# Kernel tuning notes

Measured on AMD Instinct MI355X. Metric: run time of the kernel, lower is better.

## Reference

```python
import jax, jax.numpy as jnp
import numpy as np
from jax import lax

SCALE = 2
KSIZE = 5
RGB_RANGE = 255.0
RGB_MEAN = (0.4488, 0.4371, 0.404)


def setup_inputs() -> dict:
    key = jax.random.key(0)
    ks = jax.random.split(key, 8)
    N, C, H, W = 4, 3, 128, 128
    G0 = 64
    s = SCALE
    x = jax.random.normal(ks[0], (N, C, H, W), dtype=jnp.float32)
    # relative position matrix: (1, (H*s)*(W*s), 3), values in [0,1)
    pos_mat = jax.random.uniform(ks[1], (1, H * s * W * s, 3), dtype=jnp.float32)
    conv_w = jax.random.normal(ks[2], (G0, C, KSIZE, KSIZE), dtype=jnp.float32) * 0.05
    conv_b = jax.random.normal(ks[3], (G0,), dtype=jnp.float32) * 0.05
    w1 = jax.random.normal(ks[4], (3, 256), dtype=jnp.float32) * 0.05
    b1 = jax.random.normal(ks[5], (256,), dtype=jnp.float32) * 0.05
    w2 = jax.random.normal(ks[6], (256, 9 * G0 * 3), dtype=jnp.float32) * 0.05
    b2 = jax.random.normal(ks[7], (9 * G0 * 3,), dtype=jnp.float32) * 0.05
    return {"x": x, "pos_mat": pos_mat, "conv_w": conv_w, "conv_b": conv_b,
            "w1": w1, "b1": b1, "w2": w2, "b2": b2}


def _unfold3(feat):
    # torch F.unfold(feat, 3, padding=1) ordering: channel-major then (ki, kj)
    N, C, H, W = feat.shape
    p = jnp.pad(feat, ((0, 0), (0, 0), (1, 1), (1, 1)))
    patches = jnp.stack([p[:, :, i:i + H, j:j + W]
                         for i in range(3) for j in range(3)], axis=2)  # [N,C,9,H,W]
    return patches.reshape(N, C * 9, H * W)  # [N, C*9, L]


def reference(x, pos_mat, conv_w, conv_b, w1, b1, w2, b2):
    s = SCALE
    N, _, H, W = x.shape
    # Feature extraction: conv5x5 (SAME) + ReLU
    feat = lax.conv_general_dilated(x, conv_w, (1, 1), 'SAME',
                                    dimension_numbers=('NCHW', 'OIHW', 'NCHW'))
    feat = jax.nn.relu(feat + conv_b[None, :, None, None])  # [N, G0, H, W]
    G0 = feat.shape[1]
    K = G0 * 9
    # Pos2Weight MLP: per output-pixel dynamic conv weights
    p = pos_mat.reshape(-1, 3)  # [(H*s)*(W*s), 3]
    lw = jax.nn.relu(p @ w1 + b1) @ w2 + b2  # [(H*s)*(W*s), K*3]
    # reshape to [s^2, H*W, K, 3] matching torch permute pipeline
    lw = lw.reshape(H, s, W, s, K, 3).transpose(1, 3, 0, 2, 4, 5).reshape(s * s, H * W, K, 3)
    # unfold 3x3 patches (repeat_x just tiles identical copies; compute once)
    cols = _unfold3(feat).transpose(0, 2, 1)  # [N, L, K], L = H*W
    # per-pixel matmul: out[n,p,l,c] = sum_k cols[n,l,k] * lw[p,l,k,c]
    out = jnp.einsum('nlk,plkc->nplc', cols, lw)  # [N, s^2, L, 3]
    # pixel-shuffle style rearrangement to [N, 3, H*s, W*s]
    out = out.reshape(N, s, s, H, W, 3).transpose(0, 5, 3, 1, 4, 2)
    out = out.reshape(N, 3, H * s, W * s)
    # add_mean (MeanShift sign=+1, std=1)
    mean = jnp.asarray(RGB_MEAN, dtype=out.dtype) * RGB_RANGE
    return out + mean[None, :, None, None]
```

## Files before the change

kernel.cpp:

```cpp
#include <hip/hip_runtime.h>

#define HW   128
#define OHW  256
#define G0n  64
#define HID  256
#define NOUT 1728
#define NB   4

typedef __attribute__((ext_vector_type(8))) short bf16x8;
typedef __attribute__((ext_vector_type(4))) float f32x4;
typedef __attribute__((ext_vector_type(4))) unsigned int u32x4;
typedef __attribute__((ext_vector_type(2))) unsigned int u32x2;

__device__ __forceinline__ unsigned short f2bf(float f) {
    unsigned int u = __builtin_bit_cast(unsigned int, f);
    u += 0x7fffu + ((u >> 16) & 1u);
    return (unsigned short)(u >> 16);
}
__device__ __forceinline__ float bflo(unsigned int d) {
    return __builtin_bit_cast(float, d << 16);
}
__device__ __forceinline__ float bfhi(unsigned int d) {
    return __builtin_bit_cast(float, d & 0xffff0000u);
}

__global__ __launch_bounds__(256) void prep_w2t(const float* __restrict__ w2,
                                                unsigned short* __restrict__ w2t) {
    __shared__ float t[64][65];
    int kb = blockIdx.x & 3, cb = blockIdx.x >> 2;
    int lc = threadIdx.x & 63, lr = threadIdx.x >> 6;
    #pragma unroll
    for (int i = 0; i < 16; ++i) {
        int kk = lr + i * 4;
        t[kk][lc] = w2[(kb * 64 + kk) * NOUT + cb * 64 + lc];
    }
    __syncthreads();
    #pragma unroll
    for (int i = 0; i < 16; ++i) {
        int cc = lr + i * 4;
        w2t[(cb * 64 + cc) * 256 + kb * 64 + lc] = f2bf(t[lc][cc]);
    }
}

__global__ __launch_bounds__(256) void conv5_relu_kernel(
    const float* __restrict__ x, const float* __restrict__ cw,
    const float* __restrict__ cb, float* __restrict__ feat)
{
    int idx = blockIdx.x * 256 + threadIdx.x;
    int w4 = (idx & 31) * 4;
    int h  = (idx >> 5) & 127;
    int g  = (idx >> 12) & 63;
    int n  = idx >> 18;
    float bv = cb[g];
    float a[4] = {bv, bv, bv, bv};
    const float* wp = cw + g * 75;
    #pragma unroll
    for (int ci = 0; ci < 3; ++ci) {
        const float* xr = x + (n * 3 + ci) * (HW * HW);
        #pragma unroll
        for (int ki = 0; ki < 5; ++ki) {
            int hh = h + ki - 2;
            if (hh < 0 || hh >= HW) continue;
            const float* row = xr + hh * HW;
            float f[8];
            if (w4 != 0 && w4 != 124) {
                float2 u0 = *(const float2*)(row + w4 - 2);
                float2 u1 = *(const float2*)(row + w4);
                float2 u2 = *(const float2*)(row + w4 + 2);
                float2 u3 = *(const float2*)(row + w4 + 4);
                f[0] = u0.x; f[1] = u0.y; f[2] = u1.x; f[3] = u1.y;
                f[4] = u2.x; f[5] = u2.y; f[6] = u3.x; f[7] = u3.y;
            } else {
                #pragma unroll
                for (int j = 0; j < 8; ++j) {
                    int ww = w4 - 2 + j;
                    f[j] = (ww >= 0 && ww < HW) ? row[ww] : 0.0f;
                }
            }
            float wt[5];
            #pragma unroll
            for (int kj = 0; kj < 5; ++kj) wt[kj] = wp[ci * 25 + ki * 5 + kj];
            #pragma unroll
            for (int j = 0; j < 4; ++j)
                #pragma unroll
                for (int kj = 0; kj < 5; ++kj)
                    a[j] = fmaf(f[j + kj], wt[kj], a[j]);
        }
    }
    float4 o;
    o.x = fmaxf(a[0], 0.f); o.y = fmaxf(a[1], 0.f);
    o.z = fmaxf(a[2], 0.f); o.w = fmaxf(a[3], 0.f);
    *(float4*)&feat[((n * G0n + g) * HW + h) * HW + w4] = o;
}

__global__ __launch_bounds__(256, 2) void fused_metasr_mfma(
    const float* __restrict__ feat, const unsigned short* __restrict__ w2t,
    const float* __restrict__ pos,  const float* __restrict__ w1,
    const float* __restrict__ b1,   const float* __restrict__ b2,
    float* __restrict__ out)
{
    __shared__ __align__(16) unsigned short AL[64 * 260];
    __shared__ __align__(16) unsigned short FT[64 * 6 * 4 * 8];

    const int tid = threadIdx.x;
    const int bx = blockIdx.x & 31, by = blockIdx.x >> 5;
    const int oy0 = by * 8, ox0 = bx * 8;
    const int h0 = by * 4,  w0 = bx * 4;

    for (int i = tid; i < 64 * 6 * 4 * 8; i += 256) {
        int c  = i & 7;
        int n  = (i >> 3) & 3;
        int r  = (i >> 5) % 6;
        int ci = (i >> 5) / 6;
        int gh = h0 - 1 + r, gw = w0 - 1 + c;
        float v = 0.0f;
        if (c < 6 && gh >= 0 && gh < HW && gw >= 0 && gw < HW)
            v = feat[((n * G0n + ci) * HW + gh) * HW + gw];
        FT[i] = f2bf(v);
    }

    {
        int px = tid >> 2, q = tid & 3;
        int rr = (oy0 + (px >> 3)) * OHW + (ox0 + (px & 7));
        float p0 = pos[rr * 3 + 0], p1 = pos[rr * 3 + 1], p2 = pos[rr * 3 + 2];
        #pragma unroll
        for (int j = 0; j < 16; ++j) {
            int k0 = q * 4 + j * 16;
            float4 wa = *(const float4*)&w1[k0];
            float4 wb = *(const float4*)&w1[HID + k0];
            float4 wc = *(const float4*)&w1[2 * HID + k0];
            float4 bb = *(const float4*)&b1[k0];
            unsigned short h0s = f2bf(fmaxf(fmaf(p0, wa.x, fmaf(p1, wb.x, fmaf(p2, wc.x, bb.x))), 0.f));
            unsigned short h1s = f2bf(fmaxf(fmaf(p0, wa.y, fmaf(p1, wb.y, fmaf(p2, wc.y, bb.y))), 0.f));
            unsigned short h2s = f2bf(fmaxf(fmaf(p0, wa.z, fmaf(p1, wb.z, fmaf(p2, wc.z, bb.z))), 0.f));
            unsigned short h3s = f2bf(fmaxf(fmaf(p0, wa.w, fmaf(p1, wb.w, fmaf(p2, wc.w, bb.w))), 0.f));
            u32x2 pk;
            pk.x = (unsigned)h0s | ((unsigned)h1s << 16);
            pk.y = (unsigned)h2s | ((unsigned)h3s << 16);
            *(u32x2*)&AL[px * 260 + k0] = pk;
        }
    }
    __syncthreads();

    const int lane = tid & 63, nq = tid >> 6;
    const int cl = lane & 15, hi = lane >> 4;
    bf16x8 afrag[4][8];
    #pragma unroll
    for (int m = 0; m < 4; ++m)
        #pragma unroll
        for (int k8 = 0; k8 < 8; ++k8)
            afrag[m][k8] = *(const bf16x8*)&AL[(m * 16 + cl) * 260 + k8 * 32 + hi * 8];

    const int epx = tid >> 2, en = tid & 3;
    const int iy = (epx >> 3) >> 1;
    const int ix = (epx & 7) >> 1;
    const bool selhi = (ix >= 2);
    const bool podd  = (ix & 1) != 0;
    const unsigned lwbase = (unsigned)(epx * 520);
    float oacc0 = 0.f, oacc1 = 0.f, oacc2 = 0.f;

    for (int ch = 0; ch < 9; ++ch) {
        f32x4 acc[4][3];
        #pragma unroll
        for (int m = 0; m < 4; ++m)
            #pragma unroll
            for (int j = 0; j < 3; ++j)
                acc[m][j] = (f32x4){0.f, 0.f, 0.f, 0.f};

        #pragma unroll
        for (int kh = 0; kh < 2; ++kh) {
            #pragma unroll
            for (int kk = 0; kk < 4; ++kk) {
                bf16x8 bfrag[3];
                #pragma unroll
                for (int j = 0; j < 3; ++j) {
                    int col = nq * 48 + j * 16 + cl;
                    bfrag[j] = *(const bf16x8*)&w2t[(ch * 192 + col) * 256 + kh * 128 + kk * 32 + hi * 8];
                }
                #pragma unroll
                for (int m = 0; m < 4; ++m)
                    #pragma unroll
                    for (int j = 0; j < 3; ++j)
                        acc[m][j] = __builtin_amdgcn_mfma_f32_16x16x32_bf16(
                            afrag[m][kh * 4 + kk], bfrag[j], acc[m][j], 0, 0, 0);
            }
        }

        __syncthreads();
        #pragma unroll
        for (int j = 0; j < 3; ++j) {
            int col = nq * 48 + j * 16 + cl;
            float bv = b2[ch * 192 + col];
            int kt = col / 3;
            int c  = col - kt * 3;
            #pragma unroll
            for (int m = 0; m < 4; ++m)
                #pragma unroll
                for (int r = 0; r < 4; ++r) {
                    int row = m * 16 + hi * 4 + r;
                    AL[row * 260 + kt * 4 + c] = f2bf(acc[m][j][r] + bv);
                }
        }
        __syncthreads();

        int k0 = ch * 64;
        int t3a = k0 / 3;
        int t3b = (k0 + 63) / 3;
        auto do_t3 = [&](int t3, bool guard) {
            int ci = t3 / 3;
            int di = t3 - ci * 3;
            const char* fp = (const char*)FT + ci * 384 + (iy + di) * 64 + en * 16;
            u32x4 w = *(const u32x4*)fp;
            unsigned a0 = selhi ? w.y : w.x;
            unsigned b0 = selhi ? w.z : w.y;
            float loa = bflo(a0), hia = bfhi(a0);
            float lob = bflo(b0), hib = bfhi(b0);
            float f0 = podd ? hia : loa;
            float f1 = podd ? lob : hia;
            float f2 = podd ? hib : lob;
            int ktb = 3 * t3 - k0;
            #pragma unroll
            for (int dj = 0; dj < 3; ++dj) {
                int kt = ktb + dj;
                float fv = dj == 0 ? f0 : (dj == 1 ? f1 : f2);
                if (guard) {
                    fv = ((unsigned)kt < 64u) ? fv : 0.0f;
                    kt = kt < 0 ? 0 : (kt > 63 ? 63 : kt);
                }
                u32x2 d = *(const u32x2*)((const char*)AL + lwbase + (unsigned)(kt * 8));
                oacc0 = fmaf(fv, bflo(d.x), oacc0);
                oacc1 = fmaf(fv, bfhi(d.x), oacc1);
                oacc2 = fmaf(fv, bflo(d.y), oacc2);
            }
        };
        do_t3(t3a, true);
        for (int t3 = t3a + 1; t3 < t3b; ++t3) do_t3(t3, false);
        do_t3(t3b, true);
    }

    int oy = oy0 + (epx >> 3), ox = ox0 + (epx & 7);
    out[((en * 3 + 0) * OHW + oy) * OHW + ox] = oacc0 + 0.4488f * 255.0f;
    out[((en * 3 + 1) * OHW + oy) * OHW + ox] = oacc1 + 0.4371f * 255.0f;
    out[((en * 3 + 2) * OHW + oy) * OHW + ox] = oacc2 + 0.4040f * 255.0f;
}

extern "C" void kernel_launch(void* const* d_in, const int* in_sizes, int n_in,
                              void* d_out, int out_size, void* d_ws, size_t ws_size,
                              hipStream_t stream) {
    (void)in_sizes; (void)n_in; (void)out_size; (void)ws_size;
    const float* x      = (const float*)d_in[0];
    const float* posm   = (const float*)d_in[1];
    const float* conv_w = (const float*)d_in[2];
    const float* conv_b = (const float*)d_in[3];
    const float* w1     = (const float*)d_in[4];
    const float* b1     = (const float*)d_in[5];
    const float* w2     = (const float*)d_in[6];
    const float* b2     = (const float*)d_in[7];
    float* out = (float*)d_out;

    unsigned short* w2t = (unsigned short*)d_ws;
    float* feat = (float*)((char*)d_ws + 884736);

    prep_w2t<<<108, 256, 0, stream>>>(w2, w2t);
    conv5_relu_kernel<<<(NB * G0n * HW * 32) / 256, 256, 0, stream>>>(x, conv_w, conv_b, feat);
    fused_metasr_mfma<<<1024, 256, 0, stream>>>(feat, w2t, posm, w1, b1, b2, out);
}
```

Measured before the change: 235.1 us.

## Warp-specialize fused MetaSR kernel into MFMA producer and consumer waves

Doubles the block to 512 threads. Four waves run the MFMA weight-generation GEMM and four consumer waves apply the per-pixel dynamic weights, using double-buffered LDS (AL0/AL1) so chunk ch+1's GEMM overlaps chunk ch's consumption. The feature tile is now loaded per chunk into a double-buffered slice instead of all at once, and B-fragment global loads are software-prefetched with raised wave priority around the MFMAs. This aims to hide the serialized GEMM/epilogue phases, at the cost of more LDS per block (possibly lower occupancy) and a barrier every chunk.

New measurement: 273.4 us. 1.16x slower.

```diff
diff --git a/kernel.cpp b/kernel.cpp
--- a/kernel.cpp
+++ b/kernel.cpp
@@ -93,39 +93,28 @@
     *(float4*)&feat[((n * G0n + g) * HW + h) * HW + w4] = o;
 }
 
-__global__ __launch_bounds__(256, 2) void fused_metasr_mfma(
+__global__ __launch_bounds__(512, 2) void fused_metasr_mfma(
     const float* __restrict__ feat, const unsigned short* __restrict__ w2t,
     const float* __restrict__ pos,  const float* __restrict__ w1,
     const float* __restrict__ b1,   const float* __restrict__ b2,
     float* __restrict__ out)
 {
-    __shared__ __align__(16) unsigned short AL[64 * 260];
-    __shared__ __align__(16) unsigned short FT[64 * 6 * 4 * 8];
+    __shared__ __align__(16) unsigned short AL0[64 * 260];
+    __shared__ __align__(16) unsigned short AL1[64 * 260];
+    __shared__ __align__(16) unsigned short FTS[2 * 1536];
 
     const int tid = threadIdx.x;
     const int bx = blockIdx.x & 31, by = blockIdx.x >> 5;
     const int oy0 = by * 8, ox0 = bx * 8;
     const int h0 = by * 4,  w0 = bx * 4;
 
-    for (int i = tid; i < 64 * 6 * 4 * 8; i += 256) {
-        int c  = i & 7;
-        int n  = (i >> 3) & 3;
-        int r  = (i >> 5) % 6;
-        int ci = (i >> 5) / 6;
-        int gh = h0 - 1 + r, gw = w0 - 1 + c;
-        float v = 0.0f;
-        if (c < 6 && gh >= 0 && gh < HW && gw >= 0 && gw < HW)
-            v = feat[((n * G0n + ci) * HW + gh) * HW + gw];
-        FT[i] = f2bf(v);
-    }
-
     {
-        int px = tid >> 2, q = tid & 3;
+        int px = tid >> 3, q = tid & 7;
         int rr = (oy0 + (px >> 3)) * OHW + (ox0 + (px & 7));
         float p0 = pos[rr * 3 + 0], p1 = pos[rr * 3 + 1], p2 = pos[rr * 3 + 2];
         #pragma unroll
-        for (int j = 0; j < 16; ++j) {
-            int k0 = q * 4 + j * 16;
+        for (int j = 0; j < 8; ++j) {
+            int k0 = q * 4 + j * 32;
             float4 wa = *(const float4*)&w1[k0];
             float4 wb = *(const float4*)&w1[HID + k0];
             float4 wc = *(const float4*)&w1[2 * HID + k0];
@@ -137,111 +126,141 @@
             u32x2 pk;
             pk.x = (unsigned)h0s | ((unsigned)h1s << 16);
             pk.y = (unsigned)h2s | ((unsigned)h3s << 16);
-            *(u32x2*)&AL[px * 260 + k0] = pk;
+            *(u32x2*)&AL0[px * 260 + k0] = pk;
         }
     }
     __syncthreads();
 
-    const int lane = tid & 63, nq = tid >> 6;
-    const int cl = lane & 15, hi = lane >> 4;
-    bf16x8 afrag[4][8];
-    #pragma unroll
-    for (int m = 0; m < 4; ++m)
-        #pragma unroll
-        for (int k8 = 0; k8 < 8; ++k8)
-            afrag[m][k8] = *(const bf16x8*)&AL[(m * 16 + cl) * 260 + k8 * 32 + hi * 8];
-
-    const int epx = tid >> 2, en = tid & 3;
-    const int iy = (epx >> 3) >> 1;
-    const int ix = (epx & 7) >> 1;
-    const bool selhi = (ix >= 2);
-    const bool podd  = (ix & 1) != 0;
-    const unsigned lwbase = (unsigned)(epx * 520);
-    float oacc0 = 0.f, oacc1 = 0.f, oacc2 = 0.f;
-
-    for (int ch = 0; ch < 9; ++ch) {
-        f32x4 acc[4][3];
+    const int wid = tid >> 6;
+    if (wid < 4) {
+        const int lane = tid & 63, cl = lane & 15, hi = lane >> 4;
+        const int nq = wid;
+        bf16x8 afrag[4][8];
         #pragma unroll
         for (int m = 0; m < 4; ++m)
             #pragma unroll
+            for (int k8 = 0; k8 < 8; ++k8)
+                afrag[m][k8] = *(const bf16x8*)&AL0[(m * 16 + cl) * 260 + k8 * 32 + hi * 8];
+
+        for (int ch = 0; ch < 10; ++ch) {
+            __syncthreads();
+            if (ch >= 9) continue;
+            unsigned short* lwb = (ch & 1) ? AL1 : AL0;
+            f32x4 acc[4][3];
+            #pragma unroll
+            for (int m = 0; m < 4; ++m)
+                #pragma unroll
+                for (int j = 0; j < 3; ++j)
+                    acc[m][j] = (f32x4){0.f, 0.f, 0.f, 0.f};
+
+            const unsigned short* wp = w2t + (ch * 192 + nq * 48 + cl) * 256 + hi * 8;
+            bf16x8 bfr[2][3];
+            #pragma unroll
             for (int j = 0; j < 3; ++j)
-                acc[m][j] = (f32x4){0.f, 0.f, 0.f, 0.f};
-
-        #pragma unroll
-        for (int kh = 0; kh < 2; ++kh) {
-            #pragma unroll
-            for (int kk = 0; kk < 4; ++kk) {
-                bf16x8 bfrag[3];
-                #pragma unroll
-                for (int j = 0; j < 3; ++j) {
-                    int col = nq * 48 + j * 16 + cl;
-                    bfrag[j] = *(const bf16x8*)&w2t[(ch * 192 + col) * 256 + kh * 128 + kk * 32 + hi * 8];
+                bfr[0][j] = *(const bf16x8*)(wp + j * 4096);
+            #pragma unroll
+            for (int ks = 0; ks < 8; ++ks) {
+                if (ks < 7) {
+                    #pragma unroll
+                    for (int j = 0; j < 3; ++j)
+                        bfr[(ks + 1) & 1][j] = *(const bf16x8*)(wp + j * 4096 + (ks + 1) * 32);
                 }
+                __builtin_amdgcn_s_setprio(1);
                 #pragma unroll
                 for (int m = 0; m < 4; ++m)
                     #pragma unroll
                     for (int j = 0; j < 3; ++j)
                         acc[m][j] = __builtin_amdgcn_mfma_f32_16x16x32_bf16(
-                            afrag[m][kh * 4 + kk], bfrag[j], acc[m][j], 0, 0, 0);
-            }
-        }
-
-        __syncthreads();
-        #pragma unroll
-        for (int j = 0; j < 3; ++j) {
-            int col = nq * 48 + j * 16 + cl;
-            float bv = b2[ch * 192 + col];
-            int kt = col / 3;
-            int c  = col - kt * 3;
-            #pragma unroll
-            for (int m = 0; m < 4; ++m)
-                #pragma unroll
-                for (int r = 0; r < 4; ++r) {
-                    int row = m * 16 + hi * 4 + r;
-                    AL[row * 260 + kt * 4 + c] = f2bf(acc[m][j][r] + bv);
+                            afrag[m][ks], bfr[ks & 1][j], acc[m][j], 0, 0, 0);
+                __builtin_amdgcn_s_setprio(0);
+            }
+            #pragma unroll
+            for (int j = 0; j < 3; ++j) {
+                int col = nq * 48 + j * 16 + cl;
+                float bv = b2[ch * 192 + col];
+                int kt = col / 3;
+                int c  = col - kt * 3;
+                #pragma unroll
+                for (int m = 0; m < 4; ++m)
+                    #pragma unroll
+                    for (int r = 0; r < 4; ++r)
+                        lwb[(m * 16 + hi * 4 + r) * 260 + kt * 4 + c] = f2bf(acc[m][j][r] + bv);
+            }
+        }
+    } else {
+        const int ctid = tid - 256;
+        const int epx = ctid >> 2, en = ctid & 3;
+        const int iy = (epx >> 3) >> 1;
+        const int ix = (epx & 7) >> 1;
+        const bool selhi = (ix >= 2);
+        const bool podd  = (ix & 1) != 0;
+        float oacc0 = 0.f, oacc1 = 0.f, oacc2 = 0.f;
+
+        for (int ch = 0; ch < 10; ++ch) {
+            __syncthreads();
+            if (ch < 9) {
+                int ci0 = (ch * 64) / 9;
+                unsigned short* ftb = FTS + (ch & 1) * 1536;
+                for (int i = ctid; i < 1152; i += 256) {
+                    int c = i % 6;
+                    int n = (i / 6) & 3;
+                    int r = (i / 24) % 6;
+                    int cidx = i / 144;
+                    int ci = ci0 + cidx;
+                    int gh = h0 - 1 + r, gw = w0 - 1 + c;
+                    float v = 0.0f;
+                    if (gh >= 0 && gh < HW && gw >= 0 && gw < HW)
+                        v = feat[((n * G0n + ci) * HW + gh) * HW + gw];
+                    ftb[((cidx * 6 + r) * 4 + n) * 8 + c] = f2bf(v);
                 }
-        }
-        __syncthreads();
-
-        int k0 = ch * 64;
-        int t3a = k0 / 3;
-        int t3b = (k0 + 63) / 3;
-        auto do_t3 = [&](int t3, bool guard) {
-            int ci = t3 / 3;
-            int di = t3 - ci * 3;
-            const char* fp = (const char*)FT + ci * 384 + (iy + di) * 64 + en * 16;
-            u32x4 w = *(const u32x4*)fp;
-            unsigned a0 = selhi ? w.y : w.x;
-            unsigned b0 = selhi ? w.z : w.y;
-            float loa = bflo(a0), hia = bfhi(a0);
-            float lob = bflo(b0), hib = bfhi(b0);
-            float f0 = podd ? hia : loa;
-            float f1 = podd ? lob : hia;
-            float f2 = podd ? hib : lob;
-            int ktb = 3 * t3 - k0;
-            #pragma unroll
-            for (int dj = 0; dj < 3; ++dj) {
-                int kt = ktb + dj;
-                float fv = dj == 0 ? f0 : (dj == 1 ? f1 : f2);
-                if (guard) {
-                    fv = ((unsigned)kt < 64u) ? fv : 0.0f;
-                    kt = kt < 0 ? 0 : (kt > 63 ? 63 : kt);
-                }
-                u32x2 d = *(const u32x2*)((const char*)AL + lwbase + (unsigned)(kt * 8));
-                oacc0 = fmaf(fv, bflo(d.x), oacc0);
-                oacc1 = fmaf(fv, bfhi(d.x), oacc1);
-                oacc2 = fmaf(fv, bflo(d.y), oacc2);
-            }
-        };
-        do_t3(t3a, true);
-        for (int t3 = t3a + 1; t3 < t3b; ++t3) do_t3(t3, false);
-        do_t3(t3b, true);
-    }
-
-    int oy = oy0 + (epx >> 3), ox = ox0 + (epx & 7);
-    out[((en * 3 + 0) * OHW + oy) * OHW + ox] = oacc0 + 0.4488f * 255.0f;
-    out[((en * 3 + 1) * OHW + oy) * OHW + ox] = oacc1 + 0.4371f * 255.0f;
-    out[((en * 3 + 2) * OHW + oy) * OHW + ox] = oacc2 + 0.4040f * 255.0f;
+            }
+            if (ch >= 1) {
+                int cch = ch - 1;
+                const unsigned short* lwb = (cch & 1) ? AL1 : AL0;
+                const char* ftb = (const char*)(FTS + (cch & 1) * 1536);
+                const char* lwp = (const char*)lwb + epx * 520;
+                int ci0 = (cch * 64) / 9;
+                int k0 = cch * 64;
+                int t3a = k0 / 3;
+                int t3b = (k0 + 63) / 3;
+                auto do_t3 = [&](int t3, bool guard) {
+                    int ci = t3 / 3;
+                    int di = t3 - ci * 3;
+                    const char* fp = ftb + (ci - ci0) * 384 + (iy + di) * 64 + en * 16;
+                    u32x4 w = *(const u32x4*)fp;
+                    unsigned a0 = selhi ? w.y : w.x;
+                    unsigned b0 = selhi ? w.z : w.y;
+                    float loa = bflo(a0), hia = bfhi(a0);
+                    float lob = bflo(b0), hib = bfhi(b0);
+                    float f0 = podd ? hia : loa;
+                    float f1 = podd ? lob : hia;
+                    float f2 = podd ? hib : lob;
+                    int ktb = 3 * t3 - k0;
+                    #pragma unroll
+                    for (int dj = 0; dj < 3; ++dj) {
+                        int kt = ktb + dj;
+                        float fv = dj == 0 ? f0 : (dj == 1 ? f1 : f2);
+                        if (guard) {
+                            fv = ((unsigned)kt < 64u) ? fv : 0.0f;
+                            kt = kt < 0 ? 0 : (kt > 63 ? 63 : kt);
+                        }
+                        u32x2 d = *(const u32x2*)(lwp + (unsigned)(kt * 8));
+                        oacc0 = fmaf(fv, bflo(d.x), oacc0);
+                        oacc1 = fmaf(fv, bfhi(d.x), oacc1);
+                        oacc2 = fmaf(fv, bflo(d.y), oacc2);
+                    }
+                };
+                do_t3(t3a, true);
+                for (int t3 = t3a + 1; t3 < t3b; ++t3) do_t3(t3, false);
+                do_t3(t3b, true);
+            }
+        }
+
+        int oy = oy0 + (epx >> 3), ox = ox0 + (epx & 7);
+        out[((en * 3 + 0) * OHW + oy) * OHW + ox] = oacc0 + 0.4488f * 255.0f;
+        out[((en * 3 + 1) * OHW + oy) * OHW + ox] = oacc1 + 0.4371f * 255.0f;
+        out[((en * 3 + 2) * OHW + oy) * OHW + ox] = oacc2 + 0.4040f * 255.0f;
+    }
 }
 
 extern "C" void kernel_launch(void* const* d_in, const int* in_sizes, int n_in,
@@ -263,5 +282,5 @@
 
     prep_w2t<<<108, 256, 0, stream>>>(w2, w2t);
     conv5_relu_kernel<<<(NB * G0n * HW * 32) / 256, 256, 0, stream>>>(x, conv_w, conv_b, feat);
-    fused_metasr_mfma<<<1024, 256, 0, stream>>>(feat, w2t, posm, w1, b1, b2, out);
-}
+    fused_metasr_mfma<<<1024, 512, 0, stream>>>(feat, w2t, posm, w1, b1, b2, out);
+}
```

## Split fused MetaSR block across 8 waves with halved M tiles and epilogue

Applied to the files above, without the earlier changes.

Doubles the block size to 512 threads so each wave computes two 16-row M tiles instead of four, and splits the per-pixel dynamic-conv epilogue across two lanes that are combined with a shuffle. This cuts per-thread register use (afrag, accumulators) so more waves can be resident and latency is better hidden. The cost is that each B fragment from w2t is now loaded by two waves, which doubles that global traffic, and the epilogue does extra clamped/masked iterations.

Measured after the change: 336.1 us. 1.43x slower.

```diff
diff --git a/kernel.cpp b/kernel.cpp
--- a/kernel.cpp
+++ b/kernel.cpp
@@ -93,7 +93,7 @@
     *(float4*)&feat[((n * G0n + g) * HW + h) * HW + w4] = o;
 }
 
-__global__ __launch_bounds__(256, 2) void fused_metasr_mfma(
+__global__ __launch_bounds__(512, 4) void fused_metasr_mfma(
     const float* __restrict__ feat, const unsigned short* __restrict__ w2t,
     const float* __restrict__ pos,  const float* __restrict__ w1,
     const float* __restrict__ b1,   const float* __restrict__ b2,
@@ -107,7 +107,7 @@
     const int oy0 = by * 8, ox0 = bx * 8;
     const int h0 = by * 4,  w0 = bx * 4;
 
-    for (int i = tid; i < 64 * 6 * 4 * 8; i += 256) {
+    for (int i = tid; i < 64 * 6 * 4 * 8; i += 512) {
         int c  = i & 7;
         int n  = (i >> 3) & 3;
         int r  = (i >> 5) % 6;
@@ -120,12 +120,12 @@
     }
 
     {
-        int px = tid >> 2, q = tid & 3;
+        int px = tid >> 3, q = tid & 7;
         int rr = (oy0 + (px >> 3)) * OHW + (ox0 + (px & 7));
         float p0 = pos[rr * 3 + 0], p1 = pos[rr * 3 + 1], p2 = pos[rr * 3 + 2];
         #pragma unroll
-        for (int j = 0; j < 16; ++j) {
-            int k0 = q * 4 + j * 16;
+        for (int j = 0; j < 8; ++j) {
+            int k0 = q * 32 + j * 4;
             float4 wa = *(const float4*)&w1[k0];
             float4 wb = *(const float4*)&w1[HID + k0];
             float4 wc = *(const float4*)&w1[2 * HID + k0];
@@ -142,48 +142,44 @@
     }
     __syncthreads();
 
-    const int lane = tid & 63, nq = tid >> 6;
+    const int lane = tid & 63, wid = tid >> 6;
+    const int mh = wid >> 2, nq = wid & 3;
     const int cl = lane & 15, hi = lane >> 4;
-    bf16x8 afrag[4][8];
-    #pragma unroll
-    for (int m = 0; m < 4; ++m)
+    bf16x8 afrag[2][8];
+    #pragma unroll
+    for (int m = 0; m < 2; ++m)
         #pragma unroll
         for (int k8 = 0; k8 < 8; ++k8)
-            afrag[m][k8] = *(const bf16x8*)&AL[(m * 16 + cl) * 260 + k8 * 32 + hi * 8];
-
-    const int epx = tid >> 2, en = tid & 3;
-    const int iy = (epx >> 3) >> 1;
+            afrag[m][k8] = *(const bf16x8*)&AL[(mh * 32 + m * 16 + cl) * 260 + k8 * 32 + hi * 8];
+
+    const int epx = tid >> 3, en = (tid >> 1) & 3, half = tid & 1;
+    const int iy = epx >> 4;
     const int ix = (epx & 7) >> 1;
     const bool selhi = (ix >= 2);
     const bool podd  = (ix & 1) != 0;
-    const unsigned lwbase = (unsigned)(epx * 520);
     float oacc0 = 0.f, oacc1 = 0.f, oacc2 = 0.f;
 
     for (int ch = 0; ch < 9; ++ch) {
-        f32x4 acc[4][3];
-        #pragma unroll
-        for (int m = 0; m < 4; ++m)
+        f32x4 acc[2][3];
+        #pragma unroll
+        for (int m = 0; m < 2; ++m)
             #pragma unroll
             for (int j = 0; j < 3; ++j)
                 acc[m][j] = (f32x4){0.f, 0.f, 0.f, 0.f};
-
-        #pragma unroll
-        for (int kh = 0; kh < 2; ++kh) {
-            #pragma unroll
-            for (int kk = 0; kk < 4; ++kk) {
-                bf16x8 bfrag[3];
-                #pragma unroll
-                for (int j = 0; j < 3; ++j) {
-                    int col = nq * 48 + j * 16 + cl;
-                    bfrag[j] = *(const bf16x8*)&w2t[(ch * 192 + col) * 256 + kh * 128 + kk * 32 + hi * 8];
-                }
-                #pragma unroll
-                for (int m = 0; m < 4; ++m)
-                    #pragma unroll
-                    for (int j = 0; j < 3; ++j)
-                        acc[m][j] = __builtin_amdgcn_mfma_f32_16x16x32_bf16(
-                            afrag[m][kh * 4 + kk], bfrag[j], acc[m][j], 0, 0, 0);
+        #pragma unroll
+        for (int ks = 0; ks < 8; ++ks) {
+            bf16x8 bfrag[3];
+            #pragma unroll
+            for (int j = 0; j < 3; ++j) {
+                int col = nq * 48 + j * 16 + cl;
+                bfrag[j] = *(const bf16x8*)&w2t[(ch * 192 + col) * 256 + ks * 32 + hi * 8];
             }
+            #pragma unroll
+            for (int m = 0; m < 2; ++m)
+                #pragma unroll
+                for (int j = 0; j < 3; ++j)
+                    acc[m][j] = __builtin_amdgcn_mfma_f32_16x16x32_bf16(
+                        afrag[m][ks], bfrag[j], acc[m][j], 0, 0, 0);
         }
 
         __syncthreads();
@@ -194,19 +190,19 @@
             int kt = col / 3;
             int c  = col - kt * 3;
             #pragma unroll
-            for (int m = 0; m < 4; ++m)
-                #pragma unroll
-                for (int r = 0; r < 4; ++r) {
-                    int row = m * 16 + hi * 4 + r;
-                    AL[row * 260 + kt * 4 + c] = f2bf(acc[m][j][r] + bv);
-                }
+            for (int m = 0; m < 2; ++m)
+                #pragma unroll
+                for (int r = 0; r < 4; ++r)
+                    AL[(mh * 32 + m * 16 + hi * 4 + r) * 260 + kt * 4 + c] = f2bf(acc[m][j][r] + bv);
         }
         __syncthreads();
 
-        int k0 = ch * 64;
-        int t3a = k0 / 3;
-        int t3b = (k0 + 63) / 3;
-        auto do_t3 = [&](int t3, bool guard) {
+        int k0h = ch * 64 + half * 32;
+        int t3a = k0h / 3;
+        #pragma unroll
+        for (int it = 0; it < 12; ++it) {
+            int t3 = t3a + it;
+            t3 = t3 > 191 ? 191 : t3;
             int ci = t3 / 3;
             int di = t3 - ci * 3;
             const char* fp = (const char*)FT + ci * 384 + (iy + di) * 64 + en * 16;
@@ -218,30 +214,31 @@
             float f0 = podd ? hia : loa;
             float f1 = podd ? lob : hia;
             float f2 = podd ? hib : lob;
-            int ktb = 3 * t3 - k0;
+            int kb = 3 * t3 - ch * 64;
             #pragma unroll
             for (int dj = 0; dj < 3; ++dj) {
-                int kt = ktb + dj;
+                int ktg = kb + dj;
                 float fv = dj == 0 ? f0 : (dj == 1 ? f1 : f2);
-                if (guard) {
-                    fv = ((unsigned)kt < 64u) ? fv : 0.0f;
-                    kt = kt < 0 ? 0 : (kt > 63 ? 63 : kt);
-                }
-                u32x2 d = *(const u32x2*)((const char*)AL + lwbase + (unsigned)(kt * 8));
+                unsigned rel = (unsigned)(ktg - (half << 5));
+                fv = (rel < 32u) ? fv : 0.0f;
+                int kta = ktg < 0 ? 0 : (ktg > 63 ? 63 : ktg);
+                u32x2 d = *(const u32x2*)((const char*)AL + epx * 520 + kta * 8);
                 oacc0 = fmaf(fv, bflo(d.x), oacc0);
                 oacc1 = fmaf(fv, bfhi(d.x), oacc1);
                 oacc2 = fmaf(fv, bflo(d.y), oacc2);
             }
-        };
-        do_t3(t3a, true);
-        for (int t3 = t3a + 1; t3 < t3b; ++t3) do_t3(t3, false);
-        do_t3(t3b, true);
-    }
-
-    int oy = oy0 + (epx >> 3), ox = ox0 + (epx & 7);
-    out[((en * 3 + 0) * OHW + oy) * OHW + ox] = oacc0 + 0.4488f * 255.0f;
-    out[((en * 3 + 1) * OHW + oy) * OHW + ox] = oacc1 + 0.4371f * 255.0f;
-    out[((en * 3 + 2) * OHW + oy) * OHW + ox] = oacc2 + 0.4040f * 255.0f;
+        }
+    }
+
+    oacc0 += __shfl_xor(oacc0, 1);
+    oacc1 += __shfl_xor(oacc1, 1);
+    oacc2 += __shfl_xor(oacc2, 1);
+    if (half == 0) {
+        int oy = oy0 + (epx >> 3), ox = ox0 + (epx & 7);
+        out[((en * 3 + 0) * OHW + oy) * OHW + ox] = oacc0 + 0.4488f * 255.0f;
+        out[((en * 3 + 1) * OHW + oy) * OHW + ox] = oacc1 + 0.4371f * 255.0f;
+        out[((en * 3 + 2) * OHW + oy) * OHW + ox] = oacc2 + 0.4040f * 255.0f;
+    }
 }
 
 extern "C" void kernel_launch(void* const* d_in, const int* in_sizes, int n_in,
@@ -263,5 +260,5 @@
 
     prep_w2t<<<108, 256, 0, stream>>>(w2, w2t);
     conv5_relu_kernel<<<(NB * G0n * HW * 32) / 256, 256, 0, stream>>>(x, conv_w, conv_b, feat);
-    fused_metasr_mfma<<<1024, 256, 0, stream>>>(feat, w2t, posm, w1, b1, b2, out);
-}
+    fused_metasr_mfma<<<1024, 512, 0, stream>>>(feat, w2t, posm, w1, b1, b2, out);
+}
```

## Split fused MetaSR kernel into separate weight GEMM and einsum kernels

Applied to the files above, without the earlier changes.

Splits the fused kernel in two. A GEMM kernel writes the full per-pixel dynamic weight tensor (65536 x 1728 bf16, about 226 MB) to workspace. A separate einsum kernel then reads those weights back per pixel, together with the feature tile staged in shared memory. This removes the per-chunk shared-memory round trips and block-wide barriers of the fused version, but adds a large global write and read of the weight tensor. The original fused kernel is kept as a fallback when the workspace is too small.

New measurement: 242.9 us. +3.3%, slower.

```diff
diff --git a/kernel.cpp b/kernel.cpp
--- a/kernel.cpp
+++ b/kernel.cpp
@@ -93,31 +93,16 @@
     *(float4*)&feat[((n * G0n + g) * HW + h) * HW + w4] = o;
 }
 
-__global__ __launch_bounds__(256, 2) void fused_metasr_mfma(
-    const float* __restrict__ feat, const unsigned short* __restrict__ w2t,
-    const float* __restrict__ pos,  const float* __restrict__ w1,
-    const float* __restrict__ b1,   const float* __restrict__ b2,
-    float* __restrict__ out)
+__global__ __launch_bounds__(256) void gemm_lw(
+    const unsigned short* __restrict__ w2t, const float* __restrict__ pos,
+    const float* __restrict__ w1, const float* __restrict__ b1,
+    const float* __restrict__ b2, unsigned short* __restrict__ lw)
 {
     __shared__ __align__(16) unsigned short AL[64 * 260];
-    __shared__ __align__(16) unsigned short FT[64 * 6 * 4 * 8];
 
     const int tid = threadIdx.x;
     const int bx = blockIdx.x & 31, by = blockIdx.x >> 5;
     const int oy0 = by * 8, ox0 = bx * 8;
-    const int h0 = by * 4,  w0 = bx * 4;
-
-    for (int i = tid; i < 64 * 6 * 4 * 8; i += 256) {
-        int c  = i & 7;
-        int n  = (i >> 3) & 3;
-        int r  = (i >> 5) % 6;
-        int ci = (i >> 5) / 6;
-        int gh = h0 - 1 + r, gw = w0 - 1 + c;
-        float v = 0.0f;
-        if (c < 6 && gh >= 0 && gh < HW && gw >= 0 && gw < HW)
-            v = feat[((n * G0n + ci) * HW + gh) * HW + gw];
-        FT[i] = f2bf(v);
-    }
 
     {
         int px = tid >> 2, q = tid & 3;
@@ -151,6 +136,180 @@
         for (int k8 = 0; k8 < 8; ++k8)
             afrag[m][k8] = *(const bf16x8*)&AL[(m * 16 + cl) * 260 + k8 * 32 + hi * 8];
 
+    const size_t rowbase = (size_t)blockIdx.x * 64;
+
+    for (int ch = 0; ch < 9; ++ch) {
+        f32x4 acc[4][3];
+        #pragma unroll
+        for (int m = 0; m < 4; ++m)
+            #pragma unroll
+            for (int j = 0; j < 3; ++j)
+                acc[m][j] = (f32x4){0.f, 0.f, 0.f, 0.f};
+        #pragma unroll
+        for (int ks = 0; ks < 8; ++ks) {
+            bf16x8 bfrag[3];
+            #pragma unroll
+            for (int j = 0; j < 3; ++j) {
+                int col = ch * 192 + nq * 48 + j * 16 + cl;
+                bfrag[j] = *(const bf16x8*)&w2t[(size_t)col * 256 + ks * 32 + hi * 8];
+            }
+            #pragma unroll
+            for (int m = 0; m < 4; ++m)
+                #pragma unroll
+                for (int j = 0; j < 3; ++j)
+                    acc[m][j] = __builtin_amdgcn_mfma_f32_16x16x32_bf16(
+                        afrag[m][ks], bfrag[j], acc[m][j], 0, 0, 0);
+        }
+        #pragma unroll
+        for (int j = 0; j < 3; ++j) {
+            int col = ch * 192 + nq * 48 + j * 16 + cl;
+            float bv = b2[col];
+            #pragma unroll
+            for (int m = 0; m < 4; ++m)
+                #pragma unroll
+                for (int r = 0; r < 4; ++r) {
+                    size_t row = rowbase + m * 16 + hi * 4 + r;
+                    lw[row * NOUT + col] = f2bf(acc[m][j][r] + bv);
+                }
+        }
+    }
+}
+
+__global__ __launch_bounds__(256) void einsum_out(
+    const float* __restrict__ feat, const unsigned short* __restrict__ lw,
+    float* __restrict__ out)
+{
+    __shared__ __align__(8) unsigned short FT[64 * 6 * 4 * 6];
+
+    const int tid = threadIdx.x;
+    const int bx = blockIdx.x & 31, by = blockIdx.x >> 5;
+    const int oy0 = by * 8, ox0 = bx * 8;
+    const int h0 = by * 4,  w0 = bx * 4;
+
+    for (int i = tid; i < 64 * 6 * 4 * 6; i += 256) {
+        int c = i % 6;
+        int t = i / 6;
+        int n = t & 3;
+        t >>= 2;
+        int r  = t % 6;
+        int ci = t / 6;
+        int gh = h0 - 1 + r, gw = w0 - 1 + c;
+        float v = 0.0f;
+        if (gh >= 0 && gh < HW && gw >= 0 && gw < HW)
+            v = feat[((n * G0n + ci) * HW + gh) * HW + gw];
+        FT[i] = f2bf(v);
+    }
+    __syncthreads();
+
+    const int px = tid >> 2, n = tid & 3;
+    const int iy = (px >> 3) >> 1;
+    const int ix = (px & 7) >> 1;
+    const bool podd = (ix & 1) != 0;
+    const int ixa = ix & ~1;
+
+    const u32x4* lwp = (const u32x4*)(lw + ((size_t)blockIdx.x * 64 + px) * NOUT);
+    float o0 = 0.f, o1 = 0.f, o2 = 0.f;
+
+    for (int g = 0; g < 8; ++g) {
+        u32x4 LA[14], LB[14];
+        #pragma unroll
+        for (int t = 0; t < 14; ++t) LA[t] = lwp[g * 27 + t];
+        #pragma unroll
+        for (int t = 0; t < 14; ++t) LB[t] = (t + 13 < 27) ? lwp[g * 27 + 13 + t] : (u32x4){0,0,0,0};
+
+        #pragma unroll
+        for (int cl8 = 0; cl8 < 8; ++cl8) {
+            int ci = g * 8 + cl8;
+            float fv[9];
+            #pragma unroll
+            for (int di = 0; di < 3; ++di) {
+                int rb = ((ci * 6 + iy + di) * 4 + n) * 6 + ixa;
+                unsigned u0 = *(const unsigned*)&FT[rb];
+                unsigned u1 = *(const unsigned*)&FT[rb + 2];
+                fv[di * 3 + 0] = podd ? bfhi(u0) : bflo(u0);
+                fv[di * 3 + 1] = podd ? bflo(u1) : bfhi(u0);
+                fv[di * 3 + 2] = podd ? bfhi(u1) : bflo(u1);
+            }
+            #pragma unroll
+            for (int ktl = 0; ktl < 9; ++ktl) {
+                #pragma unroll
+                for (int c = 0; c < 3; ++c) {
+                    int idx = cl8 * 27 + ktl * 3 + c;
+                    unsigned d;
+                    if (idx < 108) d = LA[idx >> 3][(idx >> 1) & 3];
+                    else { int i2 = idx - 104; d = LB[i2 >> 3][(i2 >> 1) & 3]; }
+                    float v = (idx & 1) ? bfhi(d) : bflo(d);
+                    if (c == 0) o0 = fmaf(fv[ktl], v, o0);
+                    else if (c == 1) o1 = fmaf(fv[ktl], v, o1);
+                    else o2 = fmaf(fv[ktl], v, o2);
+                }
+            }
+        }
+    }
+
+    int oy = oy0 + (px >> 3), ox = ox0 + (px & 7);
+    out[((n * 3 + 0) * OHW + oy) * OHW + ox] = o0 + 0.4488f * 255.0f;
+    out[((n * 3 + 1) * OHW + oy) * OHW + ox] = o1 + 0.4371f * 255.0f;
+    out[((n * 3 + 2) * OHW + oy) * OHW + ox] = o2 + 0.4040f * 255.0f;
+}
+
+__global__ __launch_bounds__(256, 2) void fused_metasr_mfma(
+    const float* __restrict__ feat, const unsigned short* __restrict__ w2t,
+    const float* __restrict__ pos,  const float* __restrict__ w1,
+    const float* __restrict__ b1,   const float* __restrict__ b2,
+    float* __restrict__ out)
+{
+    __shared__ __align__(16) unsigned short AL[64 * 260];
+    __shared__ __align__(16) unsigned short FT[64 * 6 * 4 * 8];
+
+    const int tid = threadIdx.x;
+    const int bx = blockIdx.x & 31, by = blockIdx.x >> 5;
+    const int oy0 = by * 8, ox0 = bx * 8;
+    const int h0 = by * 4,  w0 = bx * 4;
+
+    for (int i = tid; i < 64 * 6 * 4 * 8; i += 256) {
+        int c  = i & 7;
+        int n  = (i >> 3) & 3;
+        int r  = (i >> 5) % 6;
+        int ci = (i >> 5) / 6;
+        int gh = h0 - 1 + r, gw = w0 - 1 + c;
+        float v = 0.0f;
+        if (c < 6 && gh >= 0 && gh < HW && gw >= 0 && gw < HW)
+            v = feat[((n * G0n + ci) * HW + gh) * HW + gw];
+        FT[i] = f2bf(v);
+    }
+    {
+        int px = tid >> 2, q = tid & 3;
+        int rr = (oy0 + (px >> 3)) * OHW + (ox0 + (px & 7));
+        float p0 = pos[rr * 3 + 0], p1 = pos[rr * 3 + 1], p2 = pos[rr * 3 + 2];
+        #pragma unroll
+        for (int j = 0; j < 16; ++j) {
+            int k0 = q * 4 + j * 16;
+            float4 wa = *(const float4*)&w1[k0];
+            float4 wb = *(const float4*)&w1[HID + k0];
+            float4 wc = *(const float4*)&w1[2 * HID + k0];
+            float4 bb = *(const float4*)&b1[k0];
+            unsigned short h0s = f2bf(fmaxf(fmaf(p0, wa.x, fmaf(p1, wb.x, fmaf(p2, wc.x, bb.x))), 0.f));
+            unsigned short h1s = f2bf(fmaxf(fmaf(p0, wa.y, fmaf(p1, wb.y, fmaf(p2, wc.y, bb.y))), 0.f));
+            unsigned short h2s = f2bf(fmaxf(fmaf(p0, wa.z, fmaf(p1, wb.z, fmaf(p2, wc.z, bb.z))), 0.f));
+            unsigned short h3s = f2bf(fmaxf(fmaf(p0, wa.w, fmaf(p1, wb.w, fmaf(p2, wc.w, bb.w))), 0.f));
+            u32x2 pk;
+            pk.x = (unsigned)h0s | ((unsigned)h1s << 16);
+            pk.y = (unsigned)h2s | ((unsigned)h3s << 16);
+            *(u32x2*)&AL[px * 260 + k0] = pk;
+        }
+    }
+    __syncthreads();
+
+    const int lane = tid & 63, nq = tid >> 6;
+    const int cl = lane & 15, hi = lane >> 4;
+    bf16x8 afrag[4][8];
+    #pragma unroll
+    for (int m = 0; m < 4; ++m)
+        #pragma unroll
+        for (int k8 = 0; k8 < 8; ++k8)
+            afrag[m][k8] = *(const bf16x8*)&AL[(m * 16 + cl) * 260 + k8 * 32 + hi * 8];
+
     const int epx = tid >> 2, en = tid & 3;
     const int iy = (epx >> 3) >> 1;
     const int ix = (epx & 7) >> 1;
@@ -166,7 +325,6 @@
             #pragma unroll
             for (int j = 0; j < 3; ++j)
                 acc[m][j] = (f32x4){0.f, 0.f, 0.f, 0.f};
-
         #pragma unroll
         for (int kh = 0; kh < 2; ++kh) {
             #pragma unroll
@@ -185,7 +343,6 @@
                             afrag[m][kh * 4 + kk], bfrag[j], acc[m][j], 0, 0, 0);
             }
         }
-
         __syncthreads();
         #pragma unroll
         for (int j = 0; j < 3; ++j) {
@@ -222,15 +379,15 @@
             #pragma unroll
             for (int dj = 0; dj < 3; ++dj) {
                 int kt = ktb + dj;
-                float fv = dj == 0 ? f0 : (dj == 1 ? f1 : f2);
+                float fvv = dj == 0 ? f0 : (dj == 1 ? f1 : f2);
                 if (guard) {
-                    fv = ((unsigned)kt < 64u) ? fv : 0.0f;
+                    fvv = ((unsigned)kt < 64u) ? fvv : 0.0f;
                     kt = kt < 0 ? 0 : (kt > 63 ? 63 : kt);
                 }
                 u32x2 d = *(const u32x2*)((const char*)AL + lwbase + (unsigned)(kt * 8));
-                oacc0 = fmaf(fv, bflo(d.x), oacc0);
-                oacc1 = fmaf(fv, bfhi(d.x), oacc1);
-                oacc2 = fmaf(fv, bflo(d.y), oacc2);
+                oacc0 = fmaf(fvv, bflo(d.x), oacc0);
+                oacc1 = fmaf(fvv, bfhi(d.x), oacc1);
+                oacc2 = fmaf(fvv, bflo(d.y), oacc2);
             }
         };
         do_t3(t3a, true);
@@ -247,7 +404,7 @@
 extern "C" void kernel_launch(void* const* d_in, const int* in_sizes, int n_in,
                               void* d_out, int out_size, void* d_ws, size_t ws_size,
                               hipStream_t stream) {
-    (void)in_sizes; (void)n_in; (void)out_size; (void)ws_size;
+    (void)in_sizes; (void)n_in; (void)out_size;
     const float* x      = (const float*)d_in[0];
     const float* posm   = (const float*)d_in[1];
     const float* conv_w = (const float*)d_in[2];
@@ -260,8 +417,17 @@
 
     unsigned short* w2t = (unsigned short*)d_ws;
     float* feat = (float*)((char*)d_ws + 884736);
+    const size_t lw_off = 884736u + 16777216u;
+    const size_t lw_bytes = (size_t)65536 * NOUT * 2;
+    unsigned short* lwbuf = (unsigned short*)((char*)d_ws + lw_off);
 
     prep_w2t<<<108, 256, 0, stream>>>(w2, w2t);
     conv5_relu_kernel<<<(NB * G0n * HW * 32) / 256, 256, 0, stream>>>(x, conv_w, conv_b, feat);
-    fused_metasr_mfma<<<1024, 256, 0, stream>>>(feat, w2t, posm, w1, b1, b2, out);
-}
+
+    if (ws_size >= lw_off + lw_bytes) {
+        gemm_lw<<<1024, 256, 0, stream>>>(w2t, posm, w1, b1, b2, lwbuf);
+        einsum_out<<<1024, 256, 0, stream>>>(feat, lwbuf, out);
+    } else {
+        fused_metasr_mfma<<<1024, 256, 0, stream>>>(feat, w2t, posm, w1, b1, b2, out);
+    }
+}
```
